# Performance work log

Measured on AMD Instinct MI355X. Metric: run time of the kernel, lower is better.

The kernel has to match this reference:

```python
import jax, jax.numpy as jnp
import numpy as np

NUM_POINTS = 200_000
AMBIENT_DIM = 3
NUM_THETAS = 128
RESOLUTION = 128
BATCH_SIZE = 64


def setup_inputs() -> dict:
    key = jax.random.key(0)
    kx, kv, kb = jax.random.split(key, 3)
    x = jax.random.normal(kx, (NUM_POINTS, AMBIENT_DIM), dtype=jnp.float32)
    # unit-norm direction vectors, columns of v [ambient_dim, num_thetas]
    v = jax.random.normal(kv, (AMBIENT_DIM, NUM_THETAS), dtype=jnp.float32)
    v = v / jnp.linalg.norm(v, axis=0, keepdims=True)
    batch = jnp.sort(jax.random.randint(kb, (NUM_POINTS,), 0, BATCH_SIZE, dtype=jnp.int32))
    return {"x": x, "v": v, "batch": batch, "resolution": RESOLUTION, "batch_size": BATCH_SIZE}


def reference(x, v, batch, resolution, batch_size):
    # projected heights: [N, T]
    nh = x @ v
    N, T = nh.shape
    # bin heights over the unit ball [-1, 1] into `resolution` bins (fast ECT bincount)
    bins = jnp.clip(jnp.floor((nh + 1.0) * (0.5 * resolution)).astype(jnp.int32), 0, resolution - 1)
    theta = jnp.arange(T, dtype=jnp.int32)  # [T]
    # flat scatter index over (batch, bin, theta)
    flat = (batch.astype(jnp.int32)[:, None] * resolution + bins) * T + theta[None, :]
    hist = jnp.zeros((batch_size * resolution * T,), dtype=x.dtype)
    hist = hist.at[flat.reshape(-1)].add(1.0)
    hist = hist.reshape(batch_size, resolution, T)
    # cumulative histogram along the filtration (resolution) axis = ECT
    ect = jnp.cumsum(hist, axis=1)  # [B, resolution, num_thetas]
    return ect
```

## Files before the change

### kernel.cpp

```cpp
#include <hip/hip_runtime.h>


constexpr int N_PTS    = 200000;
constexpr int T        = 128;
constexpr int R        = 128;
constexpr int B        = 64;
constexpr int SPLIT_T  = 8;
constexpr int TT       = T / SPLIT_T;
constexpr int NTHREADS = 1024;
constexpr int TG       = 4;
constexpr int PL       = NTHREADS / TG;
constexpr int SUBS     = NTHREADS / TT;
constexpr int RCH      = R / SUBS;

__global__ __launch_bounds__(NTHREADS)
void FastEctLayer_73065983639654_kernel(const float* __restrict__ x,
                                        const float* __restrict__ v,
                                        const int*   __restrict__ batch,
                                        float*       __restrict__ out) {
    __shared__ unsigned int hist[R * TT];
    __shared__ unsigned int partial[SUBS * TT];
    __shared__ int s_range[2];

    const int tid    = threadIdx.x;
    const int tg     = tid & (TG - 1);
    const int pl     = tid >> 2;
    const int bat    = blockIdx.x / SPLIT_T;
    const int theta0 = (blockIdx.x % SPLIT_T) * TT;

    for (int i = tid; i < R * TT; i += NTHREADS) hist[i] = 0u;

    const int wave = tid >> 6, lane = tid & 63;
    if (wave < 2) {
        const int val = bat + wave;
        int lo = 0, hi = N_PTS;
        while (lo < hi) {
            const int step = (hi - lo + 63) >> 6;
            const int pos  = lo + lane * step;
            const bool pred = (pos < hi) && (batch[pos] < val);
            const unsigned long long m = __ballot(pred);
            const int k = __popcll(m);
            if (k == 0) {
                hi = lo;
            } else {
                const int nlo = lo + (k - 1) * step + 1;
                hi = min(hi, lo + k * step);
                lo = nlo;
            }
        }
        if (lane == 0) s_range[wave] = lo;
    }

    int   tlj[4];
    float vv0[4], vv1[4], vv2[4];
#pragma unroll
    for (int j = 0; j < 4; ++j) {
        const int tl = (4 * tg + j + pl) & (TT - 1);
        tlj[j] = tl;
        vv0[j] = v[0 * T + theta0 + tl];
        vv1[j] = v[1 * T + theta0 + tl];
        vv2[j] = v[2 * T + theta0 + tl];
    }

    __syncthreads();
    const int start = s_range[0];
    const int end   = s_range[1];

    const int a0      = start & ~3;
    const int nchunks = (end - a0 + 3) >> 2;
    const float4* __restrict__ X4 = (const float4*)x;
    const int cbase = (a0 >> 2) * 3;

    auto process4 = [&](int pbase, float4 f0, float4 f1, float4 f2) {
        const float px[4] = {f0.x, f0.w, f1.z, f2.y};
        const float py[4] = {f0.y, f1.x, f1.w, f2.z};
        const float pz[4] = {f0.z, f1.y, f2.x, f2.w};
        if (pbase >= start && pbase + 3 < end) {
#pragma unroll
            for (int i = 0; i < 4; ++i) {
#pragma unroll
                for (int j = 0; j < 4; ++j) {
                    const float nh = fmaf(px[i], vv0[j], fmaf(py[i], vv1[j], pz[i] * vv2[j]));
                    int bin = (int)fmaf(nh, 0.5f * (float)R, 0.5f * (float)R);
                    bin = min(max(bin, 0), R - 1);
                    atomicAdd(&hist[bin * TT + tlj[j]], 1u);
                }
            }
        } else {
#pragma unroll
            for (int i = 0; i < 4; ++i) {
                const int p = pbase + i;
                if (p >= start && p < end) {
#pragma unroll
                    for (int j = 0; j < 4; ++j) {
                        const float nh = fmaf(px[i], vv0[j], fmaf(py[i], vv1[j], pz[i] * vv2[j]));
                        int bin = (int)fmaf(nh, 0.5f * (float)R, 0.5f * (float)R);
                        bin = min(max(bin, 0), R - 1);
                        atomicAdd(&hist[bin * TT + tlj[j]], 1u);
                    }
                }
            }
        }
    };

    int c = pl;
    for (; c + PL < nchunks; c += 2 * PL) {
        const int c2 = c + PL;
        const float4 fa0 = X4[cbase + 3 * c],  fa1 = X4[cbase + 3 * c + 1],  fa2 = X4[cbase + 3 * c + 2];
        const float4 fb0 = X4[cbase + 3 * c2], fb1 = X4[cbase + 3 * c2 + 1], fb2 = X4[cbase + 3 * c2 + 2];
        process4(a0 + 4 * c,  fa0, fa1, fa2);
        process4(a0 + 4 * c2, fb0, fb1, fb2);
    }
    for (; c < nchunks; c += PL) {
        const float4 f0 = X4[cbase + 3 * c], f1 = X4[cbase + 3 * c + 1], f2 = X4[cbase + 3 * c + 2];
        process4(a0 + 4 * c, f0, f1, f2);
    }

    __syncthreads();

    const int tl  = tid & (TT - 1);
    const int sub = tid / TT;
    const int r0  = sub * RCH;
    unsigned int csum = 0;
#pragma unroll
    for (int r = r0; r < r0 + RCH; ++r) csum += hist[r * TT + tl];
    partial[sub * TT + tl] = csum;
    __syncthreads();

    unsigned int run = 0;
    for (int s = 0; s < sub; ++s) run += partial[s * TT + tl];
#pragma unroll
    for (int r = r0; r < r0 + RCH; ++r) {
        run += hist[r * TT + tl];
        out[((size_t)bat * R + r) * T + theta0 + tl] = (float)run;
    }
}

extern "C" void kernel_launch(void* const* d_in, const int* in_sizes, int n_in,
                              void* d_out, int out_size, void* d_ws, size_t ws_size,
                              hipStream_t stream) {
    const float* x     = (const float*)d_in[0];
    const float* v     = (const float*)d_in[1];
    const int*   batch = (const int*)d_in[2];
    float*       out   = (float*)d_out;

    dim3 grid(B * SPLIT_T);
    dim3 block(NTHREADS);
    hipLaunchKernelGGL(FastEctLayer_73065983639654_kernel, grid, block, 0, stream,
                       x, v, batch, out);
}
```

Before: 72.56 us.

## Duplicate LDS histograms per wave-half, fold bin scaling into directions, two-level scan

Each bin row of the shared histogram is widened to two 16-entry copies, selected by a bit of the point-lane index. Atomics from different lane groups then land on separate counters, which is meant to reduce LDS atomic contention. The direction vectors are pre-scaled by 64 so the bin comes from a single fma chain. The 2x point-unrolled loop is replaced by a simple strided loop. The final cumulative scan is restructured into 64 segments with an 8-way grouped prefix. The cost is a larger shared histogram, an extra barrier, and changed launch bounds (1024 threads, min 8 blocks), which may constrain registers.

```diff
diff --git a/kernel.cpp b/kernel.cpp
--- a/kernel.cpp
+++ b/kernel.cpp
@@ -10,16 +10,15 @@
 constexpr int NTHREADS = 1024;
 constexpr int TG       = 4;
 constexpr int PL       = NTHREADS / TG;
-constexpr int SUBS     = NTHREADS / TT;
-constexpr int RCH      = R / SUBS;
 
-__global__ __launch_bounds__(NTHREADS)
+__global__ __launch_bounds__(NTHREADS, 8)
 void FastEctLayer_73065983639654_kernel(const float* __restrict__ x,
                                         const float* __restrict__ v,
                                         const int*   __restrict__ batch,
                                         float*       __restrict__ out) {
-    __shared__ unsigned int hist[R * TT];
-    __shared__ unsigned int partial[SUBS * TT];
+    __shared__ unsigned int hist[R * 32];
+    __shared__ unsigned int partial[64 * TT];
+    __shared__ unsigned int sum8[8 * TT];
     __shared__ int s_range[2];
 
     const int tid    = threadIdx.x;
@@ -27,8 +26,9 @@
     const int pl     = tid >> 2;
     const int bat    = blockIdx.x / SPLIT_T;
     const int theta0 = (blockIdx.x % SPLIT_T) * TT;
+    const int sub16  = ((pl >> 2) & 1) << 4;
 
-    for (int i = tid; i < R * TT; i += NTHREADS) hist[i] = 0u;
+    for (int i = tid; i < R * 32; i += NTHREADS) hist[i] = 0u;
 
     const int wave = tid >> 6, lane = tid & 63;
     if (wave < 2) {
@@ -51,15 +51,15 @@
         if (lane == 0) s_range[wave] = lo;
     }
 
-    int   tlj[4];
+    int   offj[4];
     float vv0[4], vv1[4], vv2[4];
 #pragma unroll
     for (int j = 0; j < 4; ++j) {
         const int tl = (4 * tg + j + pl) & (TT - 1);
-        tlj[j] = tl;
-        vv0[j] = v[0 * T + theta0 + tl];
-        vv1[j] = v[1 * T + theta0 + tl];
-        vv2[j] = v[2 * T + theta0 + tl];
+        offj[j] = sub16 + tl;
+        vv0[j] = v[0 * T + theta0 + tl] * 64.0f;
+        vv1[j] = v[1 * T + theta0 + tl] * 64.0f;
+        vv2[j] = v[2 * T + theta0 + tl] * 64.0f;
     }
 
     __syncthreads();
@@ -80,10 +80,11 @@
             for (int i = 0; i < 4; ++i) {
 #pragma unroll
                 for (int j = 0; j < 4; ++j) {
-                    const float nh = fmaf(px[i], vv0[j], fmaf(py[i], vv1[j], pz[i] * vv2[j]));
-                    int bin = (int)fmaf(nh, 0.5f * (float)R, 0.5f * (float)R);
+                    const float bf = fmaf(px[i], vv0[j], fmaf(py[i], vv1[j],
+                                     fmaf(pz[i], vv2[j], 64.0f)));
+                    int bin = (int)bf;
                     bin = min(max(bin, 0), R - 1);
-                    atomicAdd(&hist[bin * TT + tlj[j]], 1u);
+                    atomicAdd(&hist[(bin << 5) + offj[j]], 1u);
                 }
             }
         } else {
@@ -93,45 +94,52 @@
                 if (p >= start && p < end) {
 #pragma unroll
                     for (int j = 0; j < 4; ++j) {
-                        const float nh = fmaf(px[i], vv0[j], fmaf(py[i], vv1[j], pz[i] * vv2[j]));
-                        int bin = (int)fmaf(nh, 0.5f * (float)R, 0.5f * (float)R);
+                        const float bf = fmaf(px[i], vv0[j], fmaf(py[i], vv1[j],
+                                         fmaf(pz[i], vv2[j], 64.0f)));
+                        int bin = (int)bf;
                         bin = min(max(bin, 0), R - 1);
-                        atomicAdd(&hist[bin * TT + tlj[j]], 1u);
+                        atomicAdd(&hist[(bin << 5) + offj[j]], 1u);
                     }
                 }
             }
         }
     };
 
-    int c = pl;
-    for (; c + PL < nchunks; c += 2 * PL) {
-        const int c2 = c + PL;
-        const float4 fa0 = X4[cbase + 3 * c],  fa1 = X4[cbase + 3 * c + 1],  fa2 = X4[cbase + 3 * c + 2];
-        const float4 fb0 = X4[cbase + 3 * c2], fb1 = X4[cbase + 3 * c2 + 1], fb2 = X4[cbase + 3 * c2 + 2];
-        process4(a0 + 4 * c,  fa0, fa1, fa2);
-        process4(a0 + 4 * c2, fb0, fb1, fb2);
-    }
-    for (; c < nchunks; c += PL) {
-        const float4 f0 = X4[cbase + 3 * c], f1 = X4[cbase + 3 * c + 1], f2 = X4[cbase + 3 * c + 2];
+    for (int c = pl; c < nchunks; c += PL) {
+        const float4 f0 = X4[cbase + 3 * c];
+        const float4 f1 = X4[cbase + 3 * c + 1];
+        const float4 f2 = X4[cbase + 3 * c + 2];
         process4(a0 + 4 * c, f0, f1, f2);
     }
 
     __syncthreads();
 
     const int tl  = tid & (TT - 1);
-    const int sub = tid / TT;
-    const int r0  = sub * RCH;
+    const int seg = tid >> 4;
+    const int r0  = seg * 2;
     unsigned int csum = 0;
 #pragma unroll
-    for (int r = r0; r < r0 + RCH; ++r) csum += hist[r * TT + tl];
-    partial[sub * TT + tl] = csum;
+    for (int r = r0; r < r0 + 2; ++r)
+        csum += hist[(r << 5) + tl] + hist[(r << 5) + 16 + tl];
+    partial[seg * TT + tl] = csum;
+    __syncthreads();
+
+    if (tid < 8 * TT) {
+        const int g = tid >> 4;
+        unsigned int s = 0;
+#pragma unroll
+        for (int k = 0; k < 8; ++k) s += partial[(g * 8 + k) * TT + tl];
+        sum8[g * TT + tl] = s;
+    }
     __syncthreads();
 
     unsigned int run = 0;
-    for (int s = 0; s < sub; ++s) run += partial[s * TT + tl];
+    const int g = seg >> 3;
+    for (int gg = 0; gg < g; ++gg)        run += sum8[gg * TT + tl];
+    for (int s2 = g * 8; s2 < seg; ++s2)  run += partial[s2 * TT + tl];
 #pragma unroll
-    for (int r = r0; r < r0 + RCH; ++r) {
-        run += hist[r * TT + tl];
+    for (int r = r0; r < r0 + 2; ++r) {
+        run += hist[(r << 5) + tl] + hist[(r << 5) + 16 + tl];
         out[((size_t)bat * R + r) * T + theta0 + tl] = (float)run;
     }
 }
```

Result: no change. 72.32 us (-0.3%).
